# Kernel optimization log

Hardware: AMD Instinct MI355X
Metric: run time of the kernel (lower is better)

Reference implementation:

```python
import jax, jax.numpy as jnp
import numpy as np

IN_CHANNELS = 512
NUM_HEADS = 8
PARTIAL = 4
PC = IN_CHANNELS // PARTIAL  # 128, per-branch dim


def _mha(x, wqkv, bqkv, wproj, bproj, num_heads):
    # Standard ViT-style attention block: fused qkv -> SDPA -> out proj.
    B, N, C = x.shape
    d = C // num_heads
    qkv = (x @ wqkv + bqkv).reshape(B, N, 3, num_heads, d)
    q, k, v = jnp.moveaxis(qkv, 2, 0)            # each (B, N, h, d)
    q = q.transpose(0, 2, 1, 3)                  # (B, h, N, d)
    k = k.transpose(0, 2, 1, 3)
    v = v.transpose(0, 2, 1, 3)
    scale = jnp.asarray(d, x.dtype) ** -0.5
    attn = jax.nn.softmax(jnp.einsum('bhqd,bhkd->bhqk', q, k) * scale, axis=-1)
    out = jnp.einsum('bhqk,bhkd->bhqd', attn, v)
    out = out.transpose(0, 2, 1, 3).reshape(B, N, C)
    return out @ wproj + bproj


def _channel_shuffle(x, groups):
    # ShuffleNet channel shuffle on (b, c, n, t)
    b, c, n, t = x.shape
    return x.reshape(b, groups, c // groups, n, t).transpose(0, 2, 1, 3, 4).reshape(b, c, n, t)


def setup_inputs() -> dict:
    key = jax.random.key(0)
    ks = jax.random.split(key, 13)
    b, n, t = 8, 25, 64
    inp = {'x': jax.random.normal(ks[0], (b, n, t, IN_CHANNELS), dtype=jnp.float32)}
    i = 1
    for name in ('t', 's', 'st'):
        inp[f'{name}_wqkv'] = jax.random.normal(ks[i], (PC, 3 * PC), dtype=jnp.float32) * 0.02; i += 1
        inp[f'{name}_bqkv'] = jnp.zeros((3 * PC,), dtype=jnp.float32)
        inp[f'{name}_wproj'] = jax.random.normal(ks[i], (PC, PC), dtype=jnp.float32) * 0.02; i += 1
        inp[f'{name}_bproj'] = jnp.zeros((PC,), dtype=jnp.float32)
    return inp


def reference(x, t_wqkv, t_bqkv, t_wproj, t_bproj,
              s_wqkv, s_bqkv, s_wproj, s_bproj,
              st_wqkv, st_bqkv, st_wproj, st_bproj):
    b, n, t, c = x.shape
    pc = PC
    # split order in forward: x_id, x_st, x_s, x_t (all width pc here)
    x_id = x[..., 0 * pc:1 * pc]
    x_st = x[..., 1 * pc:2 * pc]
    x_s = x[..., 2 * pc:3 * pc]
    x_t = x[..., 3 * pc:4 * pc]

    t_x = x_t.reshape(b * n, t, pc)                       # temporal: attend over t
    s_x = x_s.transpose(0, 2, 1, 3).reshape(b * t, n, pc)  # spatial: attend over n
    st_x = x_st.reshape(b, n * t, pc)                      # spatiotemporal: attend over n*t

    t_x = _mha(t_x, t_wqkv, t_bqkv, t_wproj, t_bproj, NUM_HEADS).reshape(b, n, t, pc)
    s_x = _mha(s_x, s_wqkv, s_bqkv, s_wproj, s_bproj, NUM_HEADS).reshape(b, t, n, pc).transpose(0, 2, 1, 3)
    st_x = _mha(st_x, st_wqkv, st_bqkv, st_wproj, st_bproj, NUM_HEADS).reshape(b, n, t, pc)

    # concat order: id, t, s, st (differs from split order), then to channels-first
    out = jnp.concatenate((x_id, t_x, s_x, st_x), axis=3).transpose(0, 3, 1, 2)  # (b, c, n, t)
    return _channel_shuffle(out, PARTIAL)
```

## Files before the change

kernel.cpp:

```cpp
#include <hip/hip_runtime.h>
#include <hip/hip_bf16.h>

#define BUF   1638400ull
#define QSC   0.36067376f

typedef __attribute__((ext_vector_type(4)))  float    f4;
typedef __attribute__((ext_vector_type(16))) float    f16v;
typedef __attribute__((ext_vector_type(8)))  short    s8v;
typedef __attribute__((ext_vector_type(4)))  unsigned u4v;

#if __has_builtin(__builtin_amdgcn_exp2f)
#define EXP2(x) __builtin_amdgcn_exp2f(x)
#else
#define EXP2(x) exp2f(x)
#endif
#if __has_builtin(__builtin_amdgcn_rcpf)
#define RCP(x) __builtin_amdgcn_rcpf(x)
#else
#define RCP(x) (1.0f/(x))
#endif

__device__ __forceinline__ short f2bf(float f) {
    __hip_bfloat16 h = __float2bfloat16(f);
    short s; __builtin_memcpy(&s, &h, 2); return s;
}
__device__ __forceinline__ unsigned pack2(float a, float b) {
    return (unsigned)(unsigned short)f2bf(a) | ((unsigned)(unsigned short)f2bf(b) << 16);
}
__device__ __forceinline__ float bf2f(short s) {
    return __uint_as_float((unsigned)(unsigned short)s << 16);
}
__device__ __forceinline__ unsigned tpack(float hi, float lo) {
    return __builtin_amdgcn_perm(__float_as_uint(hi), __float_as_uint(lo), 0x07060302u);
}
__device__ __forceinline__ f16v zf16() {
    f16v z;
#pragma unroll
    for (int i = 0; i < 16; i++) z[i] = 0.f;
    return z;
}

__global__ __launch_bounds__(256) void prep(
    const float* __restrict__ wq0, const float* __restrict__ wq1,
    const float* __restrict__ wq2,
    const float* __restrict__ wp0, const float* __restrict__ wp1,
    const float* __restrict__ wp2,
    short* __restrict__ wsw, short* __restrict__ onesb)
{
    const int blk = blockIdx.x, tid = threadIdx.x;
    if (blk < 96) {
        const int idx0 = blk * 2048 + tid * 8;
        const float* W; int Ncols, loc = idx0;
        if      (idx0 < 49152)  { W = wq0; Ncols = 384; }
        else if (idx0 < 98304)  { W = wq1; Ncols = 384; loc -= 49152; }
        else if (idx0 < 147456) { W = wq2; Ncols = 384; loc -= 98304; }
        else if (idx0 < 163840) { W = wp0; Ncols = 128; loc -= 147456; }
        else if (idx0 < 180224) { W = wp1; Ncols = 128; loc -= 163840; }
        else                    { W = wp2; Ncols = 128; loc -= 180224; }
        const int lane = (loc >> 3) & 63, ks = (loc >> 9) & 3, nt = loc >> 11;
        const int col = nt * 16 + (lane & 15);
        const int k0  = ks * 32 + 8 * (lane >> 4);
        s8v o;
#pragma unroll
        for (int j = 0; j < 8; j++) o[j] = f2bf(W[(k0 + j) * Ncols + col]);
        *(s8v*)(wsw + idx0) = o;
    } else {
        s8v o;
#pragma unroll
        for (int j = 0; j < 8; j++) o[j] = (short)0x3F80;
        *(s8v*)(onesb + tid * 8) = o;
    }
}

__global__ __launch_bounds__(256) void qkv_all(
    const float* __restrict__ x, const short* __restrict__ wsw,
    const float* __restrict__ bq0, const float* __restrict__ bq1,
    const float* __restrict__ bq2,
    short* __restrict__ q0, short* __restrict__ k0, short* __restrict__ vt0,
    short* __restrict__ q1, short* __restrict__ k1, short* __restrict__ vt1,
    short* __restrict__ q2, short* __restrict__ k2, short* __restrict__ vt2)
{
    const int br = blockIdx.x / 800, tile = blockIdx.x % 800;
    const int tok0 = tile * 16;
    const int wave = threadIdx.x >> 6, lane = threadIdx.x & 63;
    const int c = lane & 15, gq = lane >> 4;
    const int off = 384 - 128 * br;
    const short* wswb = wsw + br * 49152;
    const float* bias = (br == 0) ? bq0 : (br == 1) ? bq1 : bq2;

    const float* xrow = x + (size_t)(tok0 + c) * 512 + off + 8 * gq;
    s8v af[4];
#pragma unroll
    for (int ks = 0; ks < 4; ks++) {
        float4 a = *(const float4*)(xrow + ks * 32);
        float4 b = *(const float4*)(xrow + ks * 32 + 4);
        u4v t;
        t[0] = tpack(a.y, a.x); t[1] = tpack(a.w, a.z);
        t[2] = tpack(b.y, b.x); t[3] = tpack(b.w, b.z);
        af[ks] = __builtin_bit_cast(s8v, t);
    }

    const int batch0 = tok0 >> 6;
    const int b_  = tok0 / 1600;
    const int rm0 = tok0 - b_ * 1600;
    const int seq1 = rm0 >> 6;

    for (int nti = 0; nti < 6; nti++) {
        const int nt = wave * 6 + nti;
        const short* bp = wswb + ((size_t)(nt * 4) * 64 + lane) * 8;
        f4 acc = {0.f, 0.f, 0.f, 0.f};
#pragma unroll
        for (int ks = 0; ks < 4; ks++) {
            s8v bf = *(const s8v*)(bp + ks * 512);
            acc = __builtin_amdgcn_mfma_f32_16x16x32_bf16(af[ks], bf, acc, 0, 0, 0);
        }
        const float bv = bias[nt * 16 + c];
        const float v0 = acc[0]+bv, v1 = acc[1]+bv, v2 = acc[2]+bv, v3 = acc[3]+bv;
        const int which = nt >> 3, h = nt & 7;

        if (br == 0) {
            const int seq0 = (tok0 & 63) + 4 * gq;
            if (which == 2) {
                unsigned* p = (unsigned*)(vt0 + ((size_t)(batch0*8+h)*16 + c)*64 + seq0);
                p[0] = pack2(v0, v1); p[1] = pack2(v2, v3);
            } else {
                short* p = (which ? k0 : q0) + (((size_t)(batch0*8+h)*64 + seq0)*16 + c);
                p[0]=f2bf(v0); p[16]=f2bf(v1); p[32]=f2bf(v2); p[48]=f2bf(v3);
            }
        } else if (br == 1) {
            const int bt0 = b_ * 64 + (rm0 & 63) + 4 * gq;
            if (which == 2) {
                short* p = vt1 + ((size_t)(bt0*8+h)*16 + c)*32 + seq1;
                p[0]=f2bf(v0); p[4096]=f2bf(v1); p[8192]=f2bf(v2); p[12288]=f2bf(v3);
            } else {
                short* p = (which ? k1 : q1) + (((size_t)bt0*8+h)*25 + seq1)*16 + c;
                p[0]=f2bf(v0); p[3200]=f2bf(v1); p[6400]=f2bf(v2); p[9600]=f2bf(v3);
            }
        } else {
            const int seq0 = rm0 + 4 * gq;
            if (which == 2) {
                unsigned* p = (unsigned*)(vt2 + ((size_t)b_*128 + h*16 + c)*1600 + seq0);
                p[0] = pack2(v0, v1); p[1] = pack2(v2, v3);
            } else {
                short* p = (which ? k2 : q2) + (((size_t)b_*8+h)*1600 + seq0)*16 + c;
                p[0]=f2bf(v0); p[16]=f2bf(v1); p[32]=f2bf(v2); p[48]=f2bf(v3);
            }
        }
    }
}

__device__ __forceinline__ s8v load_qfrag(const short* __restrict__ qg,
                                          const int qt0, const int lane)
{
    const int n = lane & 31, g2 = lane >> 5;
    s8v qraw = *(const s8v*)(qg + (size_t)(qt0 + n) * 16 + 8 * g2);
    u4v qu;
#pragma unroll
    for (int jp = 0; jp < 4; jp++)
        qu[jp] = tpack(bf2f(qraw[2*jp+1]) * QSC, bf2f(qraw[2*jp]) * QSC);
    return __builtin_bit_cast(s8v, qu);
}

template<bool MASK>
__device__ __forceinline__ f16v attn_loop(
    const short* __restrict__ kg, const short* __restrict__ vtg, const int vstride,
    const short* __restrict__ onesb, const s8v qf, const int lane,
    const int s0, const int s1)
{
    const int n = lane & 31, g2 = lane >> 5;
    const int b4 = n >> 2;
    const int krow = ((b4 ^ (((b4 ^ (b4 >> 1)) & 1) * 3)) << 2) + (n & 3);
    const short* kp = kg + (size_t)(s0 * 32 + krow) * 16 + 8 * g2;
    const short* vp;
    int vinc;
    if (n < 16) { vp = vtg + (size_t)n * vstride + s0 * 32 + 8 * g2; vinc = 32; }
    else        { vp = onesb + 8 * g2; vinc = 0; }

    s8v kf  = *(const s8v*)kp;  kp += 512;
    s8v vf1 = *(const s8v*)vp;
    s8v vf2 = *(const s8v*)(vp + 16); vp += vinc;

    f16v oacc = zf16();
    for (int s = s0; s < s1; s++) {
        s8v kn  = *(const s8v*)kp;  kp += 512;
        s8v vn1 = *(const s8v*)vp;
        s8v vn2 = *(const s8v*)(vp + 16); vp += vinc;

        f16v sacc = __builtin_amdgcn_mfma_f32_32x32x16_bf16(kf, qf, zf16(), 0, 0, 0);

        float p[16];
#pragma unroll
        for (int r = 0; r < 16; r++) {
            p[r] = EXP2(sacc[r]);
            if (MASK && r >= 9) { if (g2) p[r] = 0.f; }
        }
        u4v u1, u2;
        u1[0]=tpack(p[1],p[0]);   u1[1]=tpack(p[3],p[2]);
        u1[2]=tpack(p[5],p[4]);   u1[3]=tpack(p[7],p[6]);
        u2[0]=tpack(p[9],p[8]);   u2[1]=tpack(p[11],p[10]);
        u2[2]=tpack(p[13],p[12]); u2[3]=tpack(p[15],p[14]);
        s8v pf1 = __builtin_bit_cast(s8v, u1);
        s8v pf2 = __builtin_bit_cast(s8v, u2);

        oacc = __builtin_amdgcn_mfma_f32_32x32x16_bf16(pf1, vf1, oacc, 0, 0, 0);
        oacc = __builtin_amdgcn_mfma_f32_32x32x16_bf16(pf2, vf2, oacc, 0, 0, 0);

        kf = kn; vf1 = vn1; vf2 = vn2;
    }
    return oacc;
}

__device__ __forceinline__ void attn_epilogue(
    const f16v oacc, short* __restrict__ obase, const int orowstride,
    const int qt0, const int nq, const int lane)
{
    const int n = lane & 31, g2 = lane >> 5;
#pragma unroll
    for (int r = 0; r < 16; r++) {
        float l = __shfl_xor(oacc[r], 16);
        float o = oacc[r] * RCP(l);
        const int q = qt0 + (r & 3) + 8 * (r >> 2) + 4 * g2;
        if (n < 16 && q < nq)
            obase[(size_t)q * orowstride + n] = f2bf(o);
    }
}

__global__ __launch_bounds__(256) void attn_all(
    const short* __restrict__ q0, const short* __restrict__ k0, const short* __restrict__ vt0,
    const short* __restrict__ q1, const short* __restrict__ k1, const short* __restrict__ vt1,
    const short* __restrict__ q2, const short* __restrict__ k2, const short* __restrict__ vt2,
    const short* __restrict__ onesb,
    short* __restrict__ ob0, short* __restrict__ ob1, short* __restrict__ ob2)
{
    __shared__ float red[4][64][17];
    const int blk = blockIdx.x;
    const int wave = threadIdx.x >> 6, lane = threadIdx.x & 63;
    const int n = lane & 31, g2 = lane >> 5;

    if (blk < 3200) {
        const int bh = blk / 50, qt0 = (blk % 50) * 32;
        const int batch = bh >> 3, h = bh & 7;
        const s8v qf = load_qfrag(q2 + (size_t)bh * 25600, qt0, lane);
        const int s0 = (50 * wave) >> 2, s1 = (50 * (wave + 1)) >> 2;
        f16v part = attn_loop<false>(
            k2 + (size_t)bh * 25600,
            vt2 + (size_t)batch * 204800 + (size_t)h * 25600, 1600,
            onesb, qf, lane, s0, s1);

#pragma unroll
        for (int j = 0; j < 16; j++) red[wave][lane][j] = part[j];
        __syncthreads();

        short* obase = ob2 + (size_t)batch * 204800 + h * 16;
#pragma unroll
        for (int j = 0; j < 4; j++) {
            const int r = 4 * wave + j;
            float sum = red[0][lane][r] + red[1][lane][r]
                      + red[2][lane][r] + red[3][lane][r];
            float l = __shfl_xor(sum, 16);
            float o = sum * RCP(l);
            const int q = qt0 + (r & 3) + 8 * (r >> 2) + 4 * g2;
            if (n < 16)
                obase[(size_t)q * 128 + n] = f2bf(o);
        }
    } else if (blk < 4000) {
        const int wid = (blk - 3200) * 4 + wave;
        const int bh = wid >> 1, qt0 = (wid & 1) * 32;
        const int bn = bh >> 3, h = bh & 7;
        const s8v qf = load_qfrag(q0 + (size_t)bh * 1024, qt0, lane);
        f16v oacc = attn_loop<false>(k0 + (size_t)bh * 1024,
                                     vt0 + (size_t)bh * 1024, 64,
                                     onesb, qf, lane, 0, 2);
        attn_epilogue(oacc, ob0 + (size_t)bn * 8192 + h * 16, 128, qt0, 64, lane);
    } else {
        const int bh = (blk - 4000) * 4 + wave;
        const int bt = bh >> 3, h = bh & 7;
        const int b_ = bt >> 6, t_ = bt & 63;
        const s8v qf = load_qfrag(q1 + (size_t)bh * 400, 0, lane);
        f16v oacc = attn_loop<true>(k1 + (size_t)bh * 400,
                                    vt1 + (size_t)bh * 512, 32,
                                    onesb, qf, lane, 0, 1);
        attn_epilogue(oacc, ob1 + (size_t)b_ * 204800 + t_ * 128 + h * 16,
                      8192, 0, 25, lane);
    }
}

__global__ __launch_bounds__(256) void projid(
    const short* __restrict__ ob0, const short* __restrict__ ob1,
    const short* __restrict__ ob2, const short* __restrict__ wsw,
    const float* __restrict__ bp0, const float* __restrict__ bp1,
    const float* __restrict__ bp2,
    const float* __restrict__ x, float* __restrict__ out)
{
    __shared__ unsigned short xl[64 * 130];
    const int blk = blockIdx.x, tid = threadIdx.x;

    if (blk < 2400) {
        const int br = blk / 800, t8 = blk % 800;
        const short* obb = (br == 0) ? ob0 : (br == 1) ? ob1 : ob2;
        const float* bp  = (br == 0) ? bp0 : (br == 1) ? bp1 : bp2;
        const short* wswb = wsw + 147456 + br * 16384;
        const int grp = br + 1;
        const int tok0 = t8 * 16;
        const int wave = tid >> 6, lane = tid & 63;
        const int c = lane & 15, gq = lane >> 4;

        s8v af[4];
#pragma unroll
        for (int ks = 0; ks < 4; ks++)
            af[ks] = *(const s8v*)(obb + (size_t)(tok0 + c) * 128 + ks * 32 + 8 * gq);

        const int bnn = t8 >> 2, b_ = bnn / 25, n_ = bnn % 25;
        const int t0 = (t8 & 3) * 16 + 4 * gq;

        for (int nti = 0; nti < 2; nti++) {
            const int nt = wave * 2 + nti;
            const short* bpw = wswb + ((size_t)(nt * 4) * 64 + lane) * 8;
            f4 acc = {0.f, 0.f, 0.f, 0.f};
#pragma unroll
            for (int ks = 0; ks < 4; ks++) {
                s8v bf = *(const s8v*)(bpw + ks * 512);
                acc = __builtin_amdgcn_mfma_f32_16x16x32_bf16(af[ks], bf, acc, 0, 0, 0);
            }
            const int c2 = nt * 16 + c;
            const float bv = bp[c2];
            float4 st = {acc[0]+bv, acc[1]+bv, acc[2]+bv, acc[3]+bv};
            *(float4*)(out + (size_t)b_ * 819200 + (size_t)(c2 * 4 + grp) * 1600
                           + n_ * 64 + t0) = st;
        }
    } else {
        const int bn = blk - 2400;
        const int b_ = bn / 25, n_ = bn % 25;
        for (int idx = tid; idx < 8192; idx += 256) {
            int row = idx >> 7, c2 = idx & 127;
            xl[row * 130 + c2] =
                (unsigned short)(__float_as_uint(x[(size_t)(bn * 64 + row) * 512 + c2]) >> 16);
        }
        __syncthreads();
        const int t_ = tid & 63, cg = tid >> 6;
        const size_t base = (size_t)b_ * 819200 + (size_t)n_ * 64 + t_;
#pragma unroll
        for (int i = 0; i < 32; i++) {
            int c2 = cg + 4 * i;
            out[base + (size_t)(c2 * 4 + 0) * 1600] =
                __uint_as_float((unsigned)xl[t_ * 130 + c2] << 16);
        }
    }
}

extern "C" void kernel_launch(void* const* d_in, const int* in_sizes, int n_in,
                              void* d_out, int out_size, void* d_ws, size_t ws_size,
                              hipStream_t stream)
{
    const float* x        = (const float*)d_in[0];
    const float* t_wqkv   = (const float*)d_in[1];
    const float* t_bqkv   = (const float*)d_in[2];
    const float* t_wproj  = (const float*)d_in[3];
    const float* t_bproj  = (const float*)d_in[4];
    const float* s_wqkv   = (const float*)d_in[5];
    const float* s_bqkv   = (const float*)d_in[6];
    const float* s_wproj  = (const float*)d_in[7];
    const float* s_bproj  = (const float*)d_in[8];
    const float* st_wqkv  = (const float*)d_in[9];
    const float* st_bqkv  = (const float*)d_in[10];
    const float* st_wproj = (const float*)d_in[11];
    const float* st_bproj = (const float*)d_in[12];

    short* wsw   = (short*)d_ws;
    short* onesb = wsw + 196608ull;
    short* q0  = onesb + 2048ull;
    short* k0  = q0 + BUF;
    short* vt0 = k0 + BUF;
    short* q1  = vt0 + BUF;
    short* k1  = q1 + BUF;
    short* vt1 = k1 + BUF;
    short* q2  = vt1 + 2097152ull;
    short* k2  = q2 + BUF;
    short* vt2 = k2 + BUF;
    short* ob0 = vt2 + BUF;
    short* ob1 = ob0 + BUF;
    short* ob2 = ob1 + BUF;
    float* out = (float*)d_out;

    prep<<<97, 256, 0, stream>>>(t_wqkv, s_wqkv, st_wqkv,
                                 t_wproj, s_wproj, st_wproj, wsw, onesb);
    qkv_all<<<2400, 256, 0, stream>>>(x, wsw, t_bqkv, s_bqkv, st_bqkv,
                                      q0, k0, vt0, q1, k1, vt1, q2, k2, vt2);
    attn_all<<<5024, 256, 0, stream>>>(q0, k0, vt0, q1, k1, vt1, q2, k2, vt2,
                                       onesb, ob0, ob1, ob2);
    projid<<<2600, 256, 0, stream>>>(ob0, ob1, ob2, wsw,
                                     t_bproj, s_bproj, st_bproj, x, out);
}
```

Baseline: 172.2 us.

## Process two query tiles per wave in spatiotemporal attention to reuse K/V loads

The spatiotemporal attention branch now has each block handle 64 queries, as two 32-row tiles per wave, instead of 32. Each K and V fragment loaded is used for both tiles, which halves K/V global traffic and the block count for that branch. The cost is higher register pressure from two accumulators and two score tiles, twice the shared memory for the reduction, and fewer blocks in the grid.

```diff
diff --git a/kernel.cpp b/kernel.cpp
--- a/kernel.cpp
+++ b/kernel.cpp
@@ -210,6 +210,59 @@
     return oacc;
 }
 
+__device__ __forceinline__ void attn_loop2(
+    const short* __restrict__ kg, const short* __restrict__ vtg, const int vstride,
+    const short* __restrict__ onesb, const s8v qfA, const s8v qfB, const int lane,
+    const int s0, const int s1, f16v& oA, f16v& oB)
+{
+    const int n = lane & 31, g2 = lane >> 5;
+    const int b4 = n >> 2;
+    const int krow = ((b4 ^ (((b4 ^ (b4 >> 1)) & 1) * 3)) << 2) + (n & 3);
+    const short* kp = kg + (size_t)(s0 * 32 + krow) * 16 + 8 * g2;
+    const short* vp;
+    int vinc;
+    if (n < 16) { vp = vtg + (size_t)n * vstride + s0 * 32 + 8 * g2; vinc = 32; }
+    else        { vp = onesb + 8 * g2; vinc = 0; }
+
+    s8v kf  = *(const s8v*)kp;  kp += 512;
+    s8v vf1 = *(const s8v*)vp;
+    s8v vf2 = *(const s8v*)(vp + 16); vp += vinc;
+
+    oA = zf16(); oB = zf16();
+    for (int s = s0; s < s1; s++) {
+        s8v kn  = *(const s8v*)kp;  kp += 512;
+        s8v vn1 = *(const s8v*)vp;
+        s8v vn2 = *(const s8v*)(vp + 16); vp += vinc;
+
+        f16v sA = __builtin_amdgcn_mfma_f32_32x32x16_bf16(kf, qfA, zf16(), 0, 0, 0);
+        f16v sB = __builtin_amdgcn_mfma_f32_32x32x16_bf16(kf, qfB, zf16(), 0, 0, 0);
+
+        float pA[16], pB[16];
+#pragma unroll
+        for (int r = 0; r < 16; r++) { pA[r] = EXP2(sA[r]); pB[r] = EXP2(sB[r]); }
+        u4v a1, a2, b1, b2;
+        a1[0]=tpack(pA[1],pA[0]);   a1[1]=tpack(pA[3],pA[2]);
+        a1[2]=tpack(pA[5],pA[4]);   a1[3]=tpack(pA[7],pA[6]);
+        a2[0]=tpack(pA[9],pA[8]);   a2[1]=tpack(pA[11],pA[10]);
+        a2[2]=tpack(pA[13],pA[12]); a2[3]=tpack(pA[15],pA[14]);
+        b1[0]=tpack(pB[1],pB[0]);   b1[1]=tpack(pB[3],pB[2]);
+        b1[2]=tpack(pB[5],pB[4]);   b1[3]=tpack(pB[7],pB[6]);
+        b2[0]=tpack(pB[9],pB[8]);   b2[1]=tpack(pB[11],pB[10]);
+        b2[2]=tpack(pB[13],pB[12]); b2[3]=tpack(pB[15],pB[14]);
+        s8v pfA1 = __builtin_bit_cast(s8v, a1);
+        s8v pfA2 = __builtin_bit_cast(s8v, a2);
+        s8v pfB1 = __builtin_bit_cast(s8v, b1);
+        s8v pfB2 = __builtin_bit_cast(s8v, b2);
+
+        oA = __builtin_amdgcn_mfma_f32_32x32x16_bf16(pfA1, vf1, oA, 0, 0, 0);
+        oB = __builtin_amdgcn_mfma_f32_32x32x16_bf16(pfB1, vf1, oB, 0, 0, 0);
+        oA = __builtin_amdgcn_mfma_f32_32x32x16_bf16(pfA2, vf2, oA, 0, 0, 0);
+        oB = __builtin_amdgcn_mfma_f32_32x32x16_bf16(pfB2, vf2, oB, 0, 0, 0);
+
+        kf = kn; vf1 = vn1; vf2 = vn2;
+    }
+}
+
 __device__ __forceinline__ void attn_epilogue(
     const f16v oacc, short* __restrict__ obase, const int orowstride,
     const int qt0, const int nq, const int lane)
@@ -232,39 +285,47 @@
     const short* __restrict__ onesb,
     short* __restrict__ ob0, short* __restrict__ ob1, short* __restrict__ ob2)
 {
-    __shared__ float red[4][64][17];
+    __shared__ float red[2][4][64][17];
     const int blk = blockIdx.x;
     const int wave = threadIdx.x >> 6, lane = threadIdx.x & 63;
     const int n = lane & 31, g2 = lane >> 5;
 
-    if (blk < 3200) {
-        const int bh = blk / 50, qt0 = (blk % 50) * 32;
+    if (blk < 1600) {
+        const int bh = blk / 25, qt0 = (blk % 25) * 64;
         const int batch = bh >> 3, h = bh & 7;
-        const s8v qf = load_qfrag(q2 + (size_t)bh * 25600, qt0, lane);
+        const short* qg = q2 + (size_t)bh * 25600;
+        const s8v qfA = load_qfrag(qg, qt0, lane);
+        const s8v qfB = load_qfrag(qg, qt0 + 32, lane);
         const int s0 = (50 * wave) >> 2, s1 = (50 * (wave + 1)) >> 2;
-        f16v part = attn_loop<false>(
-            k2 + (size_t)bh * 25600,
-            vt2 + (size_t)batch * 204800 + (size_t)h * 25600, 1600,
-            onesb, qf, lane, s0, s1);
-
-#pragma unroll
-        for (int j = 0; j < 16; j++) red[wave][lane][j] = part[j];
+        f16v pA, pB;
+        attn_loop2(k2 + (size_t)bh * 25600,
+                   vt2 + (size_t)batch * 204800 + (size_t)h * 25600, 1600,
+                   onesb, qfA, qfB, lane, s0, s1, pA, pB);
+
+#pragma unroll
+        for (int j = 0; j < 16; j++) {
+            red[0][wave][lane][j] = pA[j];
+            red[1][wave][lane][j] = pB[j];
+        }
         __syncthreads();
 
         short* obase = ob2 + (size_t)batch * 204800 + h * 16;
 #pragma unroll
-        for (int j = 0; j < 4; j++) {
-            const int r = 4 * wave + j;
-            float sum = red[0][lane][r] + red[1][lane][r]
-                      + red[2][lane][r] + red[3][lane][r];
-            float l = __shfl_xor(sum, 16);
-            float o = sum * RCP(l);
-            const int q = qt0 + (r & 3) + 8 * (r >> 2) + 4 * g2;
-            if (n < 16)
-                obase[(size_t)q * 128 + n] = f2bf(o);
-        }
-    } else if (blk < 4000) {
-        const int wid = (blk - 3200) * 4 + wave;
+        for (int qh = 0; qh < 2; qh++) {
+#pragma unroll
+            for (int j = 0; j < 4; j++) {
+                const int r = 4 * wave + j;
+                float sum = red[qh][0][lane][r] + red[qh][1][lane][r]
+                          + red[qh][2][lane][r] + red[qh][3][lane][r];
+                float l = __shfl_xor(sum, 16);
+                float o = sum * RCP(l);
+                const int q = qt0 + 32 * qh + (r & 3) + 8 * (r >> 2) + 4 * g2;
+                if (n < 16)
+                    obase[(size_t)q * 128 + n] = f2bf(o);
+            }
+        }
+    } else if (blk < 2400) {
+        const int wid = (blk - 1600) * 4 + wave;
         const int bh = wid >> 1, qt0 = (wid & 1) * 32;
         const int bn = bh >> 3, h = bh & 7;
         const s8v qf = load_qfrag(q0 + (size_t)bh * 1024, qt0, lane);
@@ -273,7 +334,7 @@
                                      onesb, qf, lane, 0, 2);
         attn_epilogue(oacc, ob0 + (size_t)bn * 8192 + h * 16, 128, qt0, 64, lane);
     } else {
-        const int bh = (blk - 4000) * 4 + wave;
+        const int bh = (blk - 2400) * 4 + wave;
         const int bt = bh >> 3, h = bh & 7;
         const int b_ = bt >> 6, t_ = bt & 63;
         const s8v qf = load_qfrag(q1 + (size_t)bh * 400, 0, lane);
@@ -386,7 +447,7 @@
                                  t_wproj, s_wproj, st_wproj, wsw, onesb);
     qkv_all<<<2400, 256, 0, stream>>>(x, wsw, t_bqkv, s_bqkv, st_bqkv,
                                       q0, k0, vt0, q1, k1, vt1, q2, k2, vt2);
-    attn_all<<<5024, 256, 0, stream>>>(q0, k0, vt0, q1, k1, vt1, q2, k2, vt2,
+    attn_all<<<3424, 256, 0, stream>>>(q0, k0, vt0, q1, k1, vt1, q2, k2, vt2,
                                        onesb, ob0, ob1, ob2);
     projid<<<2600, 256, 0, stream>>>(ob0, ob1, ob2, wsw,
                                      t_bproj, s_bproj, st_bproj, x, out);
```

After: 171.3 us. No clear change (-0.5%).
